# Kernel tuning notes

Measured on AMD Instinct MI355X. Metric: run time of the kernel, lower is better.

## Reference

```python
import jax, jax.numpy as jnp
import numpy as np

HIDDEN = 128
OUT_EMB = 256
OUT_CH = 1
NUM_LAYERS = 3
NUM_EDGES = 1000000
NUM_NODES = 50000


def glorot_orthogonal(key, shape, scale=2.0):
    # orthogonal init then rescale variance like DIG's glorot_orthogonal
    W = jax.nn.initializers.orthogonal()(key, shape, jnp.float32)
    W = W * jnp.sqrt(scale / ((shape[0] + shape[1]) * jnp.var(W)))
    return W


def setup_inputs() -> dict:
    key = jax.random.key(0)
    ks = jax.random.split(key, 8)
    e2 = jax.random.normal(ks[0], (NUM_EDGES, HIDDEN), dtype=jnp.float32)
    i = jax.random.randint(ks[1], (NUM_EDGES,), 0, NUM_NODES, dtype=jnp.int64)
    W_up = glorot_orthogonal(ks[2], (OUT_EMB, HIDDEN))
    b_up = jnp.zeros((OUT_EMB,), jnp.float32)
    Ws = jnp.stack([glorot_orthogonal(k, (OUT_EMB, OUT_EMB)) for k in jax.random.split(ks[3], NUM_LAYERS)])
    bs = jnp.zeros((NUM_LAYERS, OUT_EMB), jnp.float32)
    W_out = glorot_orthogonal(ks[4], (OUT_CH, OUT_EMB))
    return {"e2": e2, "i": i, "W_up": W_up, "b_up": b_up,
            "Ws": Ws, "bs": bs, "W_out": W_out, "num_nodes": NUM_NODES}


def reference(e2, i, W_up, b_up, Ws, bs, W_out, num_nodes):
    # scatter-sum edge messages into nodes: v[n] = sum_{k: i[k]==n} e2[k]
    v = jax.ops.segment_sum(e2, i, num_segments=num_nodes)  # [N, HIDDEN]
    v = v @ W_up.T + b_up                                   # [N, OUT_EMB]
    for l in range(NUM_LAYERS):
        v = jax.nn.silu(v @ Ws[l].T + bs[l])
    return v @ W_out.T                                      # [N, OUT_CH]
```

## Files before the change

kernel.cpp:

```cpp
#include <hip/hip_runtime.h>

#define HIDDEN 128
#define OUT_EMB 256
#define NLAYERS 3
#define TM 64
#define LDA 264

typedef __bf16 bf16x8 __attribute__((ext_vector_type(8)));
typedef float f32x4 __attribute__((ext_vector_type(4)));

__device__ __forceinline__ unsigned short f2bf(float x) {
    union { float f; unsigned u; } c; c.f = x;
    unsigned r = c.u + 0x7fff + ((c.u >> 16) & 1);
    return (unsigned short)(r >> 16);
}
__device__ __forceinline__ float bf2f(unsigned short h) {
    union { unsigned u; float f; } c; c.u = ((unsigned)h) << 16;
    return c.f;
}
__device__ __forceinline__ unsigned pack2(float a, float b) {
    return (unsigned)f2bf(a) | ((unsigned)f2bf(b) << 16);
}

__global__ __launch_bounds__(256) void hist_convert_kernel(
    const int* __restrict__ idx, int* __restrict__ counts, int ne, int nbh,
    const float* __restrict__ wup_f, const float* __restrict__ ws_f,
    unsigned short* __restrict__ wup, unsigned short* __restrict__ wsl)
{
    if ((int)blockIdx.x < nbh) {
        int e = blockIdx.x * 256 + threadIdx.x;
        if (e < ne) atomicAdd(&counts[idx[e]], 1);
    } else {
        const int n1 = OUT_EMB * HIDDEN;
        const int n2 = NLAYERS * OUT_EMB * OUT_EMB;
        int t = (blockIdx.x - nbh) * 256 + threadIdx.x;
        int base = t * 4;
        if (base < n1) {
            f32x4 x = *(const f32x4*)(wup_f + base);
            uint2 p; p.x = pack2(x[0], x[1]); p.y = pack2(x[2], x[3]);
            *(uint2*)(wup + base) = p;
        } else if (base < n1 + n2) {
            int j = base - n1;
            f32x4 x = *(const f32x4*)(ws_f + j);
            uint2 p; p.x = pack2(x[0], x[1]); p.y = pack2(x[2], x[3]);
            *(uint2*)(wsl + j) = p;
        }
    }
}

__global__ __launch_bounds__(256) void scan1_kernel(
    const int* __restrict__ counts, int* __restrict__ bsum, int n)
{
    __shared__ int sh[256];
    int t = threadIdx.x;
    int i = blockIdx.x * 256 + t;
    sh[t] = (i < n) ? counts[i] : 0;
    __syncthreads();
    for (int off = 128; off > 0; off >>= 1) {
        if (t < off) sh[t] += sh[t + off];
        __syncthreads();
    }
    if (t == 0) bsum[blockIdx.x] = sh[0];
}

__global__ __launch_bounds__(256) void scan3_kernel(
    const int* __restrict__ counts, const int* __restrict__ bsum,
    int* __restrict__ offsets, int* __restrict__ cursor, int n, int nb)
{
    __shared__ int sh[256];
    __shared__ int shb[256];
    int t = threadIdx.x;
    int i = blockIdx.x * 256 + t;
    int v  = (i < n)  ? counts[i] : 0;
    int bv = (t < nb) ? bsum[t]   : 0;
    sh[t] = v; shb[t] = bv;
    __syncthreads();
    for (int off = 1; off < 256; off <<= 1) {
        int u  = (t >= off) ? sh[t - off]  : 0;
        int ub = (t >= off) ? shb[t - off] : 0;
        __syncthreads();
        sh[t] += u; shb[t] += ub;
        __syncthreads();
    }
    if (i < n) {
        int blockoff = (blockIdx.x > 0) ? shb[blockIdx.x - 1] : 0;
        int excl = blockoff + sh[t] - v;
        offsets[i] = excl;
        cursor[i]  = excl;
    }
}

__global__ __launch_bounds__(256) void fill_kernel(
    const int* __restrict__ idx, int* __restrict__ cursor,
    int* __restrict__ edge_list, int ne)
{
    int e = blockIdx.x * 256 + threadIdx.x;
    if (e < ne) {
        int pos = atomicAdd(&cursor[idx[e]], 1);
        edge_list[pos] = e;
    }
}

__global__ __launch_bounds__(256) void gather_kernel(
    const float* __restrict__ e2, const int* __restrict__ edge_list,
    const int* __restrict__ offsets, const int* __restrict__ counts,
    unsigned short* __restrict__ vbf, int Mpad)
{
    int node = blockIdx.x * 4 + (threadIdx.x >> 6);
    if (node >= Mpad) return;
    int lane = threadIdx.x & 63;
    int half = lane >> 5;
    int c4   = lane & 31;
    int start = offsets[node];
    int cnt   = counts[node];
    const float* base = e2 + c4 * 4;

    f32x4 a0 = {0.f, 0.f, 0.f, 0.f};
    f32x4 a1 = {0.f, 0.f, 0.f, 0.f};
    f32x4 a2 = {0.f, 0.f, 0.f, 0.f};
    f32x4 a3 = {0.f, 0.f, 0.f, 0.f};

    int j = 0;
    for (; j + 8 <= cnt; j += 8) {
        int b = start + j + half * 4;
        int e0 = edge_list[b + 0];
        int e1 = edge_list[b + 1];
        int e2i = edge_list[b + 2];
        int e3 = edge_list[b + 3];
        f32x4 x0 = __builtin_nontemporal_load((const f32x4*)(base + (long long)e0  * HIDDEN));
        f32x4 x1 = __builtin_nontemporal_load((const f32x4*)(base + (long long)e1  * HIDDEN));
        f32x4 x2 = __builtin_nontemporal_load((const f32x4*)(base + (long long)e2i * HIDDEN));
        f32x4 x3 = __builtin_nontemporal_load((const f32x4*)(base + (long long)e3  * HIDDEN));
        a0 += x0;
        a1 += x1;
        a2 += x2;
        a3 += x3;
    }
    for (; j + 2 <= cnt; j += 2) {
        int e0 = edge_list[start + j + half];
        f32x4 x0 = __builtin_nontemporal_load((const f32x4*)(base + (long long)e0 * HIDDEN));
        a0 += x0;
    }
    if (j < cnt && half == 0) {
        int e0 = edge_list[start + j];
        f32x4 x0 = __builtin_nontemporal_load((const f32x4*)(base + (long long)e0 * HIDDEN));
        a1 += x0;
    }
    a0 += a2;
    a1 += a3;
    a0 += a1;
    a0[0] += __shfl_xor(a0[0], 32);
    a0[1] += __shfl_xor(a0[1], 32);
    a0[2] += __shfl_xor(a0[2], 32);
    a0[3] += __shfl_xor(a0[3], 32);

    if (half == 0) {
        uint2 p; p.x = pack2(a0[0], a0[1]); p.y = pack2(a0[2], a0[3]);
        *(uint2*)(vbf + (long long)node * HIDDEN + c4 * 4) = p;
    }
}

__global__ __launch_bounds__(256) void mlp_kernel(
    const unsigned short* __restrict__ vbf,
    const unsigned short* __restrict__ wup,
    const float* __restrict__ bup,
    const unsigned short* __restrict__ wsl,
    const float* __restrict__ bs,
    const float* __restrict__ wout,
    float* __restrict__ out, int M)
{
    __shared__ unsigned short act[TM * LDA];

    const int tid  = threadIdx.x;
    const int wv   = tid >> 6;
    const int lane = tid & 63;
    const int ln15 = lane & 15;
    const int kq   = lane >> 4;
    const int n0   = wv * 64;
    const long long rowbase = (long long)blockIdx.x * TM;

    f32x4 acc[4][4];

    #pragma unroll
    for (int mt = 0; mt < 4; ++mt)
        #pragma unroll
        for (int nt = 0; nt < 4; ++nt)
            acc[mt][nt] = (f32x4){0.f, 0.f, 0.f, 0.f};

    #pragma unroll
    for (int ks = 0; ks < 4; ++ks) {
        bf16x8 a[4], w[4];
        #pragma unroll
        for (int mt = 0; mt < 4; ++mt)
            a[mt] = *(const bf16x8*)&vbf[(rowbase + mt * 16 + ln15) * HIDDEN + ks * 32 + kq * 8];
        #pragma unroll
        for (int nt = 0; nt < 4; ++nt)
            w[nt] = *(const bf16x8*)&wup[(n0 + nt * 16 + ln15) * HIDDEN + ks * 32 + kq * 8];
        #pragma unroll
        for (int mt = 0; mt < 4; ++mt)
            #pragma unroll
            for (int nt = 0; nt < 4; ++nt)
                acc[mt][nt] = __builtin_amdgcn_mfma_f32_16x16x32_bf16(w[nt], a[mt], acc[mt][nt], 0, 0, 0);
    }
    #pragma unroll
    for (int nt = 0; nt < 4; ++nt) {
        int nb4 = n0 + nt * 16 + kq * 4;
        f32x4 bi = *(const f32x4*)(bup + nb4);
        #pragma unroll
        for (int mt = 0; mt < 4; ++mt) {
            int row = mt * 16 + ln15;
            float x0 = acc[mt][nt][0] + bi[0];
            float x1 = acc[mt][nt][1] + bi[1];
            float x2 = acc[mt][nt][2] + bi[2];
            float x3 = acc[mt][nt][3] + bi[3];
            uint2 p; p.x = pack2(x0, x1); p.y = pack2(x2, x3);
            *(uint2*)&act[row * LDA + nb4] = p;
        }
    }
    __syncthreads();

    for (int l = 0; l < NLAYERS; ++l) {
        const unsigned short* W = wsl + l * OUT_EMB * OUT_EMB;
        const float* bias_l = bs + l * OUT_EMB;

        #pragma unroll
        for (int mt = 0; mt < 4; ++mt)
            #pragma unroll
            for (int nt = 0; nt < 4; ++nt)
                acc[mt][nt] = (f32x4){0.f, 0.f, 0.f, 0.f};

        #pragma unroll
        for (int ks = 0; ks < 8; ++ks) {
            bf16x8 a[4], w[4];
            #pragma unroll
            for (int mt = 0; mt < 4; ++mt)
                a[mt] = *(const bf16x8*)&act[(mt * 16 + ln15) * LDA + ks * 32 + kq * 8];
            #pragma unroll
            for (int nt = 0; nt < 4; ++nt)
                w[nt] = *(const bf16x8*)&W[(n0 + nt * 16 + ln15) * OUT_EMB + ks * 32 + kq * 8];
            #pragma unroll
            for (int mt = 0; mt < 4; ++mt)
                #pragma unroll
                for (int nt = 0; nt < 4; ++nt)
                    acc[mt][nt] = __builtin_amdgcn_mfma_f32_16x16x32_bf16(w[nt], a[mt], acc[mt][nt], 0, 0, 0);
        }
        __syncthreads();
        #pragma unroll
        for (int nt = 0; nt < 4; ++nt) {
            int nb4 = n0 + nt * 16 + kq * 4;
            f32x4 bi = *(const f32x4*)(bias_l + nb4);
            #pragma unroll
            for (int mt = 0; mt < 4; ++mt) {
                int row = mt * 16 + ln15;
                float x0 = acc[mt][nt][0] + bi[0];
                float x1 = acc[mt][nt][1] + bi[1];
                float x2 = acc[mt][nt][2] + bi[2];
                float x3 = acc[mt][nt][3] + bi[3];
                x0 = x0 * __builtin_amdgcn_rcpf(1.f + __expf(-x0));
                x1 = x1 * __builtin_amdgcn_rcpf(1.f + __expf(-x1));
                x2 = x2 * __builtin_amdgcn_rcpf(1.f + __expf(-x2));
                x3 = x3 * __builtin_amdgcn_rcpf(1.f + __expf(-x3));
                uint2 p; p.x = pack2(x0, x1); p.y = pack2(x2, x3);
                *(uint2*)&act[row * LDA + nb4] = p;
            }
        }
        __syncthreads();
    }

    {
        int r = tid >> 2;
        int part = tid & 3;
        const unsigned short* arow = &act[r * LDA + part * 64];
        const float* wrow = wout + part * 64;
        float s = 0.f;
        #pragma unroll
        for (int jj = 0; jj < 8; ++jj) {
            bf16x8 v = *(const bf16x8*)&arow[jj * 8];
            f32x4 w0 = *(const f32x4*)&wrow[jj * 8];
            f32x4 w1 = *(const f32x4*)&wrow[jj * 8 + 4];
            s += (float)v[0] * w0[0] + (float)v[1] * w0[1]
               + (float)v[2] * w0[2] + (float)v[3] * w0[3]
               + (float)v[4] * w1[0] + (float)v[5] * w1[1]
               + (float)v[6] * w1[2] + (float)v[7] * w1[3];
        }
        s += __shfl_xor(s, 1);
        s += __shfl_xor(s, 2);
        long long rowg = rowbase + r;
        if (part == 0 && rowg < M) out[rowg] = s;
    }
}

extern "C" void kernel_launch(void* const* d_in, const int* in_sizes, int n_in,
                              void* d_out, int out_size, void* d_ws, size_t ws_size,
                              hipStream_t stream) {
    const float* e2    = (const float*)d_in[0];
    const int*   idx   = (const int*)d_in[1];
    const float* W_up  = (const float*)d_in[2];
    const float* b_up  = (const float*)d_in[3];
    const float* Ws    = (const float*)d_in[4];
    const float* bs    = (const float*)d_in[5];
    const float* W_out = (const float*)d_in[6];

    const int ne = in_sizes[0] / HIDDEN;
    const int M  = out_size;
    const int Mpad = ((M + TM - 1) / TM) * TM;
    const int nb = (Mpad + 255) / 256;

    char* p = (char*)d_ws;
    unsigned short* vbf    = (unsigned short*)p;  p += (size_t)Mpad * HIDDEN * 2;
    unsigned short* wup_bf = (unsigned short*)p;  p += (size_t)OUT_EMB * HIDDEN * 2;
    unsigned short* wsl_bf = (unsigned short*)p;  p += (size_t)NLAYERS * OUT_EMB * OUT_EMB * 2;
    int* counts    = (int*)p;  p += (size_t)Mpad * 4;
    int* offsets   = (int*)p;  p += (size_t)Mpad * 4;
    int* cursor    = (int*)p;  p += (size_t)Mpad * 4;
    int* bsum      = (int*)p;  p += 256 * 4;
    int* edge_list = (int*)p;  p += (size_t)ne * 4;

    hipMemsetAsync(counts, 0, (size_t)Mpad * 4, stream);

    {
        const int nbh = (ne + 255) / 256;
        const int total4 = (OUT_EMB * HIDDEN + NLAYERS * OUT_EMB * OUT_EMB) / 4;
        const int nbc = (total4 + 255) / 256;
        hist_convert_kernel<<<nbh + nbc, 256, 0, stream>>>(
            idx, counts, ne, nbh, W_up, Ws, wup_bf, wsl_bf);
    }
    scan1_kernel<<<nb, 256, 0, stream>>>(counts, bsum, Mpad);
    scan3_kernel<<<nb, 256, 0, stream>>>(counts, bsum, offsets, cursor, Mpad, nb);
    fill_kernel <<<(ne + 255) / 256, 256, 0, stream>>>(idx, cursor, edge_list, ne);

    gather_kernel<<<(Mpad + 3) / 4, 256, 0, stream>>>(e2, edge_list, offsets, counts, vbf, Mpad);

    mlp_kernel<<<Mpad / TM, 256, 0, stream>>>(vbf, wup_bf, b_up, wsl_bf, bs, W_out,
                                              (float*)d_out, M);
}
```

Before: 849.8 us.

## Fuse edge gather into MLP kernel, staging node sums in shared memory

Merges the gather/segment-sum kernel into the MLP kernel. Each 64-row block now accumulates its own node rows into LDS instead of writing a bf16 intermediate to global memory and reading it back. This removes one launch and the intermediate round trip. In exchange, the gather runs with far fewer blocks (Mpad/64 instead of Mpad/4) and only 4 waves per block, which lowers memory-level parallelism for the bandwidth-bound gather. Each block also serializes 16 nodes per wave.

Measured after the change: 903.0 us. 1.06x slower.

```diff
diff --git a/kernel.cpp b/kernel.cpp
--- a/kernel.cpp
+++ b/kernel.cpp
@@ -5,6 +5,7 @@
 #define NLAYERS 3
 #define TM 64
 #define LDA 264
+#define LDV 136
 
 typedef __bf16 bf16x8 __attribute__((ext_vector_type(8)));
 typedef float f32x4 __attribute__((ext_vector_type(4)));
@@ -13,10 +14,6 @@
     union { float f; unsigned u; } c; c.f = x;
     unsigned r = c.u + 0x7fff + ((c.u >> 16) & 1);
     return (unsigned short)(r >> 16);
-}
-__device__ __forceinline__ float bf2f(unsigned short h) {
-    union { unsigned u; float f; } c; c.u = ((unsigned)h) << 16;
-    return c.f;
 }
 __device__ __forceinline__ unsigned pack2(float a, float b) {
     return (unsigned)f2bf(a) | ((unsigned)f2bf(b) << 16);
@@ -101,67 +98,9 @@
     }
 }
 
-__global__ __launch_bounds__(256) void gather_kernel(
+__global__ __launch_bounds__(256) void gmlp_kernel(
     const float* __restrict__ e2, const int* __restrict__ edge_list,
     const int* __restrict__ offsets, const int* __restrict__ counts,
-    unsigned short* __restrict__ vbf, int Mpad)
-{
-    int node = blockIdx.x * 4 + (threadIdx.x >> 6);
-    if (node >= Mpad) return;
-    int lane = threadIdx.x & 63;
-    int half = lane >> 5;
-    int c4   = lane & 31;
-    int start = offsets[node];
-    int cnt   = counts[node];
-    const float* base = e2 + c4 * 4;
-
-    f32x4 a0 = {0.f, 0.f, 0.f, 0.f};
-    f32x4 a1 = {0.f, 0.f, 0.f, 0.f};
-    f32x4 a2 = {0.f, 0.f, 0.f, 0.f};
-    f32x4 a3 = {0.f, 0.f, 0.f, 0.f};
-
-    int j = 0;
-    for (; j + 8 <= cnt; j += 8) {
-        int b = start + j + half * 4;
-        int e0 = edge_list[b + 0];
-        int e1 = edge_list[b + 1];
-        int e2i = edge_list[b + 2];
-        int e3 = edge_list[b + 3];
-        f32x4 x0 = __builtin_nontemporal_load((const f32x4*)(base + (long long)e0  * HIDDEN));
-        f32x4 x1 = __builtin_nontemporal_load((const f32x4*)(base + (long long)e1  * HIDDEN));
-        f32x4 x2 = __builtin_nontemporal_load((const f32x4*)(base + (long long)e2i * HIDDEN));
-        f32x4 x3 = __builtin_nontemporal_load((const f32x4*)(base + (long long)e3  * HIDDEN));
-        a0 += x0;
-        a1 += x1;
-        a2 += x2;
-        a3 += x3;
-    }
-    for (; j + 2 <= cnt; j += 2) {
-        int e0 = edge_list[start + j + half];
-        f32x4 x0 = __builtin_nontemporal_load((const f32x4*)(base + (long long)e0 * HIDDEN));
-        a0 += x0;
-    }
-    if (j < cnt && half == 0) {
-        int e0 = edge_list[start + j];
-        f32x4 x0 = __builtin_nontemporal_load((const f32x4*)(base + (long long)e0 * HIDDEN));
-        a1 += x0;
-    }
-    a0 += a2;
-    a1 += a3;
-    a0 += a1;
-    a0[0] += __shfl_xor(a0[0], 32);
-    a0[1] += __shfl_xor(a0[1], 32);
-    a0[2] += __shfl_xor(a0[2], 32);
-    a0[3] += __shfl_xor(a0[3], 32);
-
-    if (half == 0) {
-        uint2 p; p.x = pack2(a0[0], a0[1]); p.y = pack2(a0[2], a0[3]);
-        *(uint2*)(vbf + (long long)node * HIDDEN + c4 * 4) = p;
-    }
-}
-
-__global__ __launch_bounds__(256) void mlp_kernel(
-    const unsigned short* __restrict__ vbf,
     const unsigned short* __restrict__ wup,
     const float* __restrict__ bup,
     const unsigned short* __restrict__ wsl,
@@ -169,16 +108,61 @@
     const float* __restrict__ wout,
     float* __restrict__ out, int M)
 {
-    __shared__ unsigned short act[TM * LDA];
+    __shared__ __align__(16) unsigned short act[TM * LDA];
+    unsigned short* vrow = act;
 
     const int tid  = threadIdx.x;
     const int wv   = tid >> 6;
     const int lane = tid & 63;
+    const int half = lane >> 5;
+    const int c4   = lane & 31;
     const int ln15 = lane & 15;
     const int kq   = lane >> 4;
     const int n0   = wv * 64;
     const long long rowbase = (long long)blockIdx.x * TM;
 
+    {
+        const float* basep = e2 + c4 * 4;
+        #pragma unroll 1
+        for (int k = 0; k < 16; ++k) {
+            int node  = (int)rowbase + wv * 16 + k;
+            int start = offsets[node];
+            int cnt   = counts[node];
+            f32x4 a0 = {0.f,0.f,0.f,0.f}, a1 = {0.f,0.f,0.f,0.f};
+            f32x4 a2 = {0.f,0.f,0.f,0.f}, a3 = {0.f,0.f,0.f,0.f};
+            int j = 0;
+            for (; j + 8 <= cnt; j += 8) {
+                int b = start + j + half * 4;
+                int e0  = edge_list[b + 0];
+                int e1  = edge_list[b + 1];
+                int e2i = edge_list[b + 2];
+                int e3  = edge_list[b + 3];
+                a0 += __builtin_nontemporal_load((const f32x4*)(basep + (long long)e0  * HIDDEN));
+                a1 += __builtin_nontemporal_load((const f32x4*)(basep + (long long)e1  * HIDDEN));
+                a2 += __builtin_nontemporal_load((const f32x4*)(basep + (long long)e2i * HIDDEN));
+                a3 += __builtin_nontemporal_load((const f32x4*)(basep + (long long)e3  * HIDDEN));
+            }
+            for (; j + 2 <= cnt; j += 2) {
+                int e0 = edge_list[start + j + half];
+                a0 += __builtin_nontemporal_load((const f32x4*)(basep + (long long)e0 * HIDDEN));
+            }
+            if (j < cnt && half == 0) {
+                int e0 = edge_list[start + j];
+                a1 += __builtin_nontemporal_load((const f32x4*)(basep + (long long)e0 * HIDDEN));
+            }
+            a0 += a2; a1 += a3; a0 += a1;
+            a0[0] += __shfl_xor(a0[0], 32);
+            a0[1] += __shfl_xor(a0[1], 32);
+            a0[2] += __shfl_xor(a0[2], 32);
+            a0[3] += __shfl_xor(a0[3], 32);
+            if (half == 0) {
+                uint2 p; p.x = pack2(a0[0], a0[1]); p.y = pack2(a0[2], a0[3]);
+                *(uint2*)&vrow[(wv * 16 + k) * LDV + c4 * 4] = p;
+            }
+        }
+    }
+    __syncthreads();
+
     f32x4 acc[4][4];
 
     #pragma unroll
@@ -192,7 +176,7 @@
         bf16x8 a[4], w[4];
         #pragma unroll
         for (int mt = 0; mt < 4; ++mt)
-            a[mt] = *(const bf16x8*)&vbf[(rowbase + mt * 16 + ln15) * HIDDEN + ks * 32 + kq * 8];
+            a[mt] = *(const bf16x8*)&vrow[(mt * 16 + ln15) * LDV + ks * 32 + kq * 8];
         #pragma unroll
         for (int nt = 0; nt < 4; ++nt)
             w[nt] = *(const bf16x8*)&wup[(n0 + nt * 16 + ln15) * HIDDEN + ks * 32 + kq * 8];
@@ -202,6 +186,7 @@
             for (int nt = 0; nt < 4; ++nt)
                 acc[mt][nt] = __builtin_amdgcn_mfma_f32_16x16x32_bf16(w[nt], a[mt], acc[mt][nt], 0, 0, 0);
     }
+    __syncthreads();
     #pragma unroll
     for (int nt = 0; nt < 4; ++nt) {
         int nb4 = n0 + nt * 16 + kq * 4;
@@ -248,7 +233,7 @@
         #pragma unroll
         for (int nt = 0; nt < 4; ++nt) {
             int nb4 = n0 + nt * 16 + kq * 4;
-            f32x4 bi = *(const f32x4*)(bias_l + nb4);
+            f32x4 bi = *(const f32x4*)(bs + l * OUT_EMB + nb4);
             #pragma unroll
             for (int mt = 0; mt < 4; ++mt) {
                 int row = mt * 16 + ln15;
@@ -265,6 +250,7 @@
             }
         }
         __syncthreads();
+        (void)bias_l;
     }
 
     {
@@ -307,7 +293,6 @@
     const int nb = (Mpad + 255) / 256;
 
     char* p = (char*)d_ws;
-    unsigned short* vbf    = (unsigned short*)p;  p += (size_t)Mpad * HIDDEN * 2;
     unsigned short* wup_bf = (unsigned short*)p;  p += (size_t)OUT_EMB * HIDDEN * 2;
     unsigned short* wsl_bf = (unsigned short*)p;  p += (size_t)NLAYERS * OUT_EMB * OUT_EMB * 2;
     int* counts    = (int*)p;  p += (size_t)Mpad * 4;
@@ -329,8 +314,7 @@
     scan3_kernel<<<nb, 256, 0, stream>>>(counts, bsum, offsets, cursor, Mpad, nb);
     fill_kernel <<<(ne + 255) / 256, 256, 0, stream>>>(idx, cursor, edge_list, ne);
 
-    gather_kernel<<<(Mpad + 3) / 4, 256, 0, stream>>>(e2, edge_list, offsets, counts, vbf, Mpad);
-
-    mlp_kernel<<<Mpad / TM, 256, 0, stream>>>(vbf, wup_bf, b_up, wsl_bf, bs, W_out,
-                                              (float*)d_out, M);
-}
+    gmlp_kernel<<<Mpad / TM, 256, 0, stream>>>(e2, edge_list, offsets, counts,
+                                               wup_bf, b_up, wsl_bf, bs, W_out,
+                                               (float*)d_out, M);
+}
```
